# Kernel tuning notes

Hardware: AMD Instinct MI355X
Metric: run time of the kernel (lower is better)

## Reference

```python
import jax, jax.numpy as jnp
import numpy as np
from jax import lax

DIM = 64
HEADS = 8

def conv1x1(x, w):
    # x: [B,C,H,W], w: [O,I,1,1]
    return lax.conv_general_dilated(x, w, (1, 1), 'VALID',
                                    dimension_numbers=('NCHW', 'OIHW', 'NCHW'))

def dwconv3x3(x, w):
    # depthwise 3x3, w: [C,1,3,3]
    C = x.shape[1]
    return lax.conv_general_dilated(x, w, (1, 1), ((1, 1), (1, 1)),
                                    dimension_numbers=('NCHW', 'OIHW', 'NCHW'),
                                    feature_group_count=C)

def setup_inputs() -> dict:
    key = jax.random.key(0)
    ks = jax.random.split(key, 7)
    B, C, H, W = 8, DIM, 256, 256
    x = jax.random.normal(ks[0], (B, C, H, W), dtype=jnp.float32)
    w_gate = jax.random.normal(ks[1], (C, C, 1, 1), dtype=jnp.float32) * 0.05
    w_gate_dw = jax.random.normal(ks[2], (C, 1, 3, 3), dtype=jnp.float32) * 0.05
    w_qkv = jax.random.normal(ks[3], (3 * C, C, 1, 1), dtype=jnp.float32) * 0.05
    w_qkv_dw = jax.random.normal(ks[4], (3 * C, 1, 3, 3), dtype=jnp.float32) * 0.05
    w_proj = jax.random.normal(ks[5], (C, C, 1, 1), dtype=jnp.float32) * 0.05
    temperature = jnp.ones((HEADS, 1, 1), dtype=jnp.float32)
    return {'x': x, 'w_gate': w_gate, 'w_gate_dw': w_gate_dw,
            'w_qkv': w_qkv, 'w_qkv_dw': w_qkv_dw, 'w_proj': w_proj,
            'temperature': temperature}

def reference(x, w_gate, w_gate_dw, w_qkv, w_qkv_dw, w_proj, temperature):
    b, c, h, w = x.shape
    head = HEADS
    cph = c // head  # channels per head

    gate = dwconv3x3(conv1x1(x, w_gate), w_gate_dw)  # [b,c,h,w]
    qkv = dwconv3x3(conv1x1(x, w_qkv), w_qkv_dw)     # [b,3c,h,w]
    q, k, v = jnp.split(qkv, 3, axis=1)

    def to_heads(t):
        return t.reshape(b, head, cph, h * w)  # [b,head,c',hw]
    q, k, v = to_heads(q), to_heads(k), to_heads(v)

    # L2-normalize along the spatial (hw) axis (torch F.normalize, eps=1e-12)
    q = q / jnp.maximum(jnp.linalg.norm(q, axis=-1, keepdims=True), 1e-12)
    k = k / jnp.maximum(jnp.linalg.norm(k, axis=-1, keepdims=True), 1e-12)

    # transposed attention over channels: [b,head,c',c']
    attn = jnp.einsum('bhcn,bhdn->bhcd', q, k) * temperature
    attn = jax.nn.softmax(attn, axis=-1)
    out = jnp.einsum('bhcd,bhdn->bhcn', attn, v)  # [b,head,c',hw]
    out = out.reshape(b, c, h, w)

    out = jax.nn.gelu(gate, approximate=False) * out
    out = conv1x1(out, w_proj)
    return out
```

## Files before the change

### kernel.cpp

```cpp
#include <hip/hip_runtime.h>

typedef _Float16 f16;
using f16x4 = __attribute__((ext_vector_type(4))) _Float16;
using f16x8 = __attribute__((ext_vector_type(8))) _Float16;
using f32x4 = __attribute__((ext_vector_type(4))) float;

#define HW 65536
#define NBAND 16
#define ROWS 16
#define RS 320

static __device__ __forceinline__ float my_erf(float v) {
  float x = fabsf(v);
  float t = 1.f / (1.f + 0.3275911f * x);
  float y = t * (0.254829592f + t * (-0.284496736f + t * (1.421413741f
          + t * (-1.453152027f + t * 1.061405429f))));
  float r = 1.f - y * __expf(-x * x);
  return v < 0.f ? -r : r;
}
static __device__ __forceinline__ float my_gelu(float s) {
  return 0.5f * s * (1.f + my_erf(s * 0.70710678118654752f));
}

__global__ void TRA_Attention_15281493639325_kernel() {}

__global__ void k_signal(float* out, long long n, float val) {
  long long i = (long long)blockIdx.x * blockDim.x + threadIdx.x;
  long long stride = (long long)gridDim.x * blockDim.x;
  for (; i < n; i += stride) out[i] = val;
}

__global__ __launch_bounds__(256) void k0_wconv(
    const float* __restrict__ w_gate, const float* __restrict__ w_qkv,
    f16* __restrict__ W16)
{
  int i = blockIdx.x * 256 + threadIdx.x;
  int m = i >> 4, kc = i & 15;
  const float* src = (m < 64) ? (w_gate + m*64 + kc*4)
                              : (w_qkv + (m-64)*64 + kc*4);
  float4 f = *(const float4*)src;
  f16x4 pk = { (f16)f.x, (f16)f.y, (f16)f.z, (f16)f.w };
  *(f16x4*)(W16 + m*64 + kc*4) = pk;
}

__global__ __launch_bounds__(256) void k1_mfma(
    const float* __restrict__ x, const f16* __restrict__ W16,
    f16* __restrict__ A)
{
  __shared__ __align__(16) unsigned char xs[8192];
  __shared__ __align__(16) f16 os[256*64];

  const int tid = threadIdx.x, blk = blockIdx.x;
  const int b = blk >> 8;
  const long long row0 = (long long)(blk & 255) * 256;

  const int wave = tid >> 6, lane = tid & 63;
  const int m0 = (wave >> 1) * 128, n0 = (wave & 1) * 32;
  const int lr = lane & 15, lg = lane >> 4;

  float4 pre[4];
  #pragma unroll
  for (int i = 0; i < 4; ++i) {
    int cid = tid + (i << 8), k = cid >> 4, c = cid & 15;
    pre[i] = *(const float4*)(x + ((long long)b*64 + k)*HW + row0 + c*4);
  }

  for (int t = 0; t < 4; ++t) {
    const long long p0 = row0 + t*64;

    #pragma unroll
    for (int i = 0; i < 4; ++i) {
      int cid = tid + (i << 8), k = cid >> 4, c = cid & 15;
      const float* e = (const float*)&pre[i];
      #pragma unroll
      for (int j = 0; j < 4; ++j) {
        int p = c*4 + j;
        int hp = ((p & 7) ^ ((p >> 3) & 7)) << 4;
        *(f16*)(xs + p*128 + ((2*k) ^ hp)) = (f16)e[j];
      }
    }
    __syncthreads();

    if (t < 3) {
      const long long pn = row0 + (t+1)*64;
      #pragma unroll
      for (int i = 0; i < 4; ++i) {
        int cid = tid + (i << 8), k = cid >> 4, c = cid & 15;
        pre[i] = *(const float4*)(x + ((long long)b*64 + k)*HW + pn + c*4);
      }
    }

    f32x4 acc[8][2];
    #pragma unroll
    for (int i = 0; i < 8; ++i)
      #pragma unroll
      for (int j = 0; j < 2; ++j) acc[i][j] = (f32x4){0.f,0.f,0.f,0.f};

    #pragma unroll
    for (int ks = 0; ks < 2; ++ks) {
      f16x8 af[8], bfr[2];
      #pragma unroll
      for (int mi = 0; mi < 8; ++mi) {
        int m = m0 + mi*16 + lr;
        af[mi] = *(const f16x8*)(W16 + m*64 + ks*32 + lg*8);
      }
      #pragma unroll
      for (int ni = 0; ni < 2; ++ni) {
        int p = n0 + ni*16 + lr;
        int hp = ((p & 7) ^ ((p >> 3) & 7)) << 4;
        bfr[ni] = *(const f16x8*)(xs + p*128 + ((ks*64 + lg*16) ^ hp));
      }
      #pragma unroll
      for (int mi = 0; mi < 8; ++mi)
        #pragma unroll
        for (int ni = 0; ni < 2; ++ni)
          acc[mi][ni] = __builtin_amdgcn_mfma_f32_16x16x32_f16(
              af[mi], bfr[ni], acc[mi][ni], 0, 0, 0);
    }
    __syncthreads();

    #pragma unroll
    for (int mi = 0; mi < 8; ++mi)
      #pragma unroll
      for (int ni = 0; ni < 2; ++ni)
        #pragma unroll
        for (int r = 0; r < 4; ++r) {
          int m = m0 + mi*16 + lg*4 + r;
          int p = n0 + ni*16 + lr;
          os[m*64 + (p ^ ((m & 7) << 3))] = (f16)acc[mi][ni][r];
        }
    __syncthreads();

    #pragma unroll
    for (int pass = 0; pass < 8; ++pass) {
      int idx = pass*256 + tid;
      int row = idx >> 3, c8 = idx & 7;
      f16x8 v = *(const f16x8*)((const unsigned char*)os + row*128
                                + ((c8 ^ (row & 7)) * 16));
      *(f16x8*)(A + ((long long)b*256 + row)*HW + p0 + c8*8) = v;
    }
    __syncthreads();
  }
}

__global__ __launch_bounds__(256) void k2a_dw(
    const f16* __restrict__ A, const float* __restrict__ w_gate_dw,
    const float* __restrict__ w_qkv_dw, f16* __restrict__ Vv, f16* __restrict__ GG)
{
  const int tid = threadIdx.x, blk = blockIdx.x;
  const int yband = blk & 3, ch2 = (blk >> 2) & 127, b = blk >> 9;
  const bool isv = ch2 >= 64;
  const int c = isv ? ch2 - 64 : ch2;
  const f16* src = A + ((long long)b*256 + (isv ? 192 + c : c)) * HW;
  const float* wsrc = isv ? (w_qkv_dw + (128 + c)*9) : (w_gate_dw + c*9);
  f16* dst = (isv ? Vv : GG) + ((long long)b*64 + c) * HW;

  float wd[9];
  #pragma unroll
  for (int j = 0; j < 9; ++j) wd[j] = wsrc[j];

  const int xc = tid & 31, ysub = tid >> 5;
  const int lane = tid & 63;
  const int xbase = xc * 8;
  const int y0 = yband * 64 + ysub * 8;

  float rb[3][10];

  auto load_row = [&](int y, float* r) {
    if (y >= 0 && y < 256) {
      uint4 raw = *(const uint4*)(src + y*256 + xbase);
      const f16* e = (const f16*)&raw;
      #pragma unroll
      for (int t = 0; t < 8; ++t) r[1 + t] = (float)e[t];
    } else {
      #pragma unroll
      for (int t = 0; t < 8; ++t) r[1 + t] = 0.f;
    }
    float lf = __shfl(r[8], lane - 1);
    float rf = __shfl(r[1], lane + 1);
    r[0] = (xc == 0)  ? 0.f : lf;
    r[9] = (xc == 31) ? 0.f : rf;
  };

  load_row(y0 - 1, rb[0]);
  load_row(y0,     rb[1]);

  #pragma unroll
  for (int i = 0; i < 8; ++i) {
    load_row(y0 + i + 1, rb[(i + 2) % 3]);
    const float* rm = rb[i % 3];
    const float* r0 = rb[(i + 1) % 3];
    const float* rp = rb[(i + 2) % 3];
    f16x8 st;
    #pragma unroll
    for (int j = 0; j < 8; ++j) {
      float s = wd[0]*rm[j] + wd[1]*rm[j+1] + wd[2]*rm[j+2]
              + wd[3]*r0[j] + wd[4]*r0[j+1] + wd[5]*r0[j+2]
              + wd[6]*rp[j] + wd[7]*rp[j+1] + wd[8]*rp[j+2];
      if (!isv) s = my_gelu(s);
      st[j] = (f16)s;
    }
    *(f16x8*)(dst + (y0 + i)*256 + xbase) = st;
  }
}

__device__ __forceinline__ int ridx(int c, int slot, int i) {
  return ((((c << 2) | slot) * RS) + i) ^ ((c & 7) << 3);
}

__global__ __launch_bounds__(64) void k2b_qk(
    const f16* __restrict__ A, const float* __restrict__ w_qkv_dw,
    float* __restrict__ GRP)
{
  __shared__ __align__(16) f16 ring[16*4*RS];
  const int lane = threadIdx.x, blk = blockIdx.x;
  const int band = blk & (NBAND-1), h = (blk >> 4) & 7, b = blk >> 7;

  const int c  = lane & 15, g  = lane >> 4;
  const int cs = lane >> 2, q4 = lane & 3;

  const int wrow = (c < 8) ? (h*8 + c) : (64 + h*8 + (c - 8));
  float wq[9];
  #pragma unroll
  for (int j = 0; j < 9; ++j) wq[j] = w_qkv_dw[wrow*9 + j];

  const f16* sbase = A + ((long long)b*256 +
      (cs < 8 ? 64 + h*8 + cs : 128 + h*8 + (cs - 8))) * HW;

  ring[ridx(cs, q4, 7)]   = (f16)0.f;
  ring[ridx(cs, q4, 264)] = (f16)0.f;

  auto load_row = [&](int yy, uint4* r) {
    if (yy >= 0 && yy < 256) {
      const f16* p = sbase + yy*256 + q4*64;
      #pragma unroll
      for (int t = 0; t < 8; ++t) r[t] = *(const uint4*)(p + t*8);
    } else {
      #pragma unroll
      for (int t = 0; t < 8; ++t) r[t] = make_uint4(0u,0u,0u,0u);
    }
  };
  auto write_row = [&](int slot, const uint4* r) {
    #pragma unroll
    for (int t = 0; t < 8; ++t)
      *(uint4*)&ring[ridx(cs, slot, 8 + q4*64 + t*8)] = r[t];
  };

  const int y0 = band * ROWS;
  {
    uint4 r[8];
    load_row(y0-1, r); write_row((y0+3)&3, r);
    load_row(y0,   r); write_row((y0+4)&3, r);
    load_row(y0+1, r); write_row((y0+5)&3, r);
  }
  __syncthreads();

  f32x4 acc = (f32x4){0.f, 0.f, 0.f, 0.f};

  for (int y = y0; y < y0 + ROWS; ++y) {
    uint4 r[8];
    const bool pf = (y + 2 <= y0 + ROWS);
    if (pf) load_row(y + 2, r);

    const int s0 = (y+3)&3, s1 = (y+4)&3, s2 = (y+5)&3;
    #pragma unroll
    for (int q = 0; q < 8; ++q) {
      const int base = 7 + q*32 + g*8;
      float v0[10], v1[10], v2[10];
      #pragma unroll
      for (int t = 0; t < 10; ++t) {
        v0[t] = (float)ring[ridx(c, s0, base+t)];
        v1[t] = (float)ring[ridx(c, s1, base+t)];
        v2[t] = (float)ring[ridx(c, s2, base+t)];
      }
      f16x8 frag;
      #pragma unroll
      for (int j = 0; j < 8; ++j) {
        float s = wq[0]*v0[j] + wq[1]*v0[j+1] + wq[2]*v0[j+2]
                + wq[3]*v1[j] + wq[4]*v1[j+1] + wq[5]*v1[j+2]
                + wq[6]*v2[j] + wq[7]*v2[j+1] + wq[8]*v2[j+2];
        frag[j] = (f16)s;
      }
      acc = __builtin_amdgcn_mfma_f32_16x16x32_f16(frag, frag, acc, 0, 0, 0);
    }
    if (pf) write_row((y+6)&3, r);
    __syncthreads();
  }

  const long long gbase = (long long)((b*8 + h)*NBAND + band) * 80;
  #pragma unroll
  for (int reg = 0; reg < 4; ++reg) {
    int rrow = g*4 + reg;
    float val = acc[reg];
    if (rrow == c) GRP[gbase + c] = val;
    else if (rrow < 8 && c >= 8) GRP[gbase + 16 + rrow*8 + (c-8)] = val;
  }
}

__global__ __launch_bounds__(64) void k2c_attn(
    const float* __restrict__ GRP, const float* __restrict__ temp,
    float* __restrict__ ATT)
{
  __shared__ float s[80];
  const int tid = threadIdx.x;
  const int h = blockIdx.x & 7, b = blockIdx.x >> 3;
  for (int i = tid; i < 80; i += 64) {
    float v = 0.f;
    for (int band = 0; band < NBAND; ++band)
      v += GRP[(((b*8 + h)*NBAND + band) * 80) + i];
    s[i] = v;
  }
  __syncthreads();
  const int c = tid >> 3, d = tid & 7;
  float nq = fmaxf(sqrtf(s[c]), 1e-12f);
  float nk = fmaxf(sqrtf(s[8 + d]), 1e-12f);
  float logit = s[16 + c*8 + d] / (nq * nk) * temp[h];
  float m = logit;
  #pragma unroll
  for (int off = 4; off; off >>= 1) m = fmaxf(m, __shfl_xor(m, off));
  float e = __expf(logit - m);
  float sum = e;
  #pragma unroll
  for (int off = 4; off; off >>= 1) sum += __shfl_xor(sum, off);
  ATT[((b*8 + h)*8 + c)*8 + d] = e / sum;
}

__global__ __launch_bounds__(256) void k3_out(
    const f16* __restrict__ Vv, const f16* __restrict__ GG,
    const float* __restrict__ ATT, const float* __restrict__ w_proj,
    float* __restrict__ out)
{
  __shared__ __align__(16) unsigned char lds[64*128 + 256*128 + 2048];
  unsigned char* wl = lds;
  unsigned char* xs = lds + 64*128;
  float* attn_s = (float*)(lds + 64*128 + 256*128);

  const int tid = threadIdx.x;
  const int y = blockIdx.x & 255, b = blockIdx.x >> 8;

  for (int cid = tid; cid < 1024; cid += 256) {
    int m = cid >> 4, kc = cid & 15;
    float4 f = *(const float4*)(w_proj + m*64 + kc*4);
    int hm = ((m & 7) ^ ((m >> 3) & 7)) << 4;
    f16x4 pk = { (f16)f.x, (f16)f.y, (f16)f.z, (f16)f.w };
    *(f16x4*)(wl + m*128 + ((kc*8) ^ hm)) = pk;
  }
  for (int i = tid; i < 512; i += 256) attn_s[i] = ATT[b*512 + i];
  __syncthreads();

  {
    const int pg = tid & 31, hd = tid >> 5;
    const long long base = ((long long)b*64 + hd*8)*HW + (long long)y*256 + pg*8;
    f16x8 vv[8], gg[8];
    #pragma unroll
    for (int d = 0; d < 8; ++d)
      vv[d] = *(const f16x8*)(Vv + base + (long long)d*HW);
    #pragma unroll
    for (int c = 0; c < 8; ++c)
      gg[c] = *(const f16x8*)(GG + base + (long long)c*HW);
    float a[8][8];
    #pragma unroll
    for (int c = 0; c < 8; ++c)
      #pragma unroll
      for (int d = 0; d < 8; ++d) a[c][d] = attn_s[hd*64 + c*8 + d];
    #pragma unroll
    for (int j = 0; j < 8; ++j) {
      int p = pg*8 + j;
      int hp = ((p & 7) ^ ((p >> 3) & 7)) << 4;
      f16x8 st;
      #pragma unroll
      for (int c = 0; c < 8; ++c) {
        float av = 0.f;
        #pragma unroll
        for (int d = 0; d < 8; ++d) av += a[c][d] * (float)vv[d][j];
        st[c] = (f16)((float)gg[c][j] * av);
      }
      *(f16x8*)(xs + p*128 + ((hd*16) ^ hp)) = st;
    }
  }
  __syncthreads();

  const int wave = tid >> 6, lane = tid & 63;
  const int n0 = wave * 64;
  const int lr = lane & 15, lg = lane >> 4;

  f32x4 acc[4][4];
  #pragma unroll
  for (int i = 0; i < 4; ++i)
    #pragma unroll
    for (int j = 0; j < 4; ++j) acc[i][j] = (f32x4){0.f,0.f,0.f,0.f};

  #pragma unroll
  for (int ks = 0; ks < 2; ++ks) {
    f16x8 af[4], bfr[4];
    #pragma unroll
    for (int mi = 0; mi < 4; ++mi) {
      int m = mi*16 + lr;
      int hm = ((m & 7) ^ ((m >> 3) & 7)) << 4;
      af[mi] = *(const f16x8*)(wl + m*128 + ((ks*64 + lg*16) ^ hm));
    }
    #pragma unroll
    for (int ni = 0; ni < 4; ++ni) {
      int p = n0 + ni*16 + lr;
      int hp = ((p & 7) ^ ((p >> 3) & 7)) << 4;
      bfr[ni] = *(const f16x8*)(xs + p*128 + ((ks*64 + lg*16) ^ hp));
    }
    #pragma unroll
    for (int mi = 0; mi < 4; ++mi)
      #pragma unroll
      for (int ni = 0; ni < 4; ++ni)
        acc[mi][ni] = __builtin_amdgcn_mfma_f32_16x16x32_f16(
            af[mi], bfr[ni], acc[mi][ni], 0, 0, 0);
  }

  const long long obase = (long long)b*64*HW + (long long)y*256;
  #pragma unroll
  for (int mi = 0; mi < 4; ++mi)
    #pragma unroll
    for (int ni = 0; ni < 4; ++ni)
      #pragma unroll
      for (int r = 0; r < 4; ++r) {
        int m = mi*16 + lg*4 + r;
        int p = n0 + ni*16 + lr;
        out[obase + (long long)m*HW + p] = acc[mi][ni][r];
      }
}

extern "C" void kernel_launch(void* const* d_in, const int* in_sizes, int n_in,
                              void* d_out, int out_size, void* d_ws, size_t ws_size,
                              hipStream_t stream)
{
  float* out = (float*)d_out;

  int mp[7] = {-1,-1,-1,-1,-1,-1,-1};
  bool ok = (n_in == 7);
  if (ok) {
    int n4 = 0;
    for (int i = 0; i < 7; ++i) {
      long s = in_sizes[i];
      if      (s == 33554432) mp[0] = i;
      else if (s == 576)      mp[2] = i;
      else if (s == 12288)    mp[3] = i;
      else if (s == 1728)     mp[4] = i;
      else if (s == 8)        mp[6] = i;
      else if (s == 4096)     { if (n4 == 0) mp[1] = i; else mp[5] = i; ++n4; }
    }
    ok = ok && (n4 == 2);
    for (int i = 0; i < 7; ++i) ok = ok && (mp[i] >= 0);
  }
  if (!ok) { k_signal<<<2048,256,0,stream>>>(out, (long long)out_size, 2000.0f); return; }
  if (out_size != 33554432) { k_signal<<<2048,256,0,stream>>>(out, (long long)out_size, 3000.0f); return; }

  const float* x    = (const float*)d_in[mp[0]];
  const float* wg   = (const float*)d_in[mp[1]];
  const float* wgd  = (const float*)d_in[mp[2]];
  const float* wqkv = (const float*)d_in[mp[3]];
  const float* wqd  = (const float*)d_in[mp[4]];
  const float* wpj  = (const float*)d_in[mp[5]];
  const float* tp   = (const float*)d_in[mp[6]];

  unsigned char* ws = (unsigned char*)d_ws;
  const size_t GRP_SZ   = 8UL*8*NBAND*80*4;
  const size_t FULL     = 402653184UL + GRP_SZ + 16384UL + 32768UL;
  const size_t PERB_GRP = 8UL*NBAND*80*4;
  const size_t PERB     = 50331648UL + PERB_GRP + 2048UL + 32768UL;

  if (ws != nullptr && ws_size >= FULL) {
    f16*   A    = (f16*)ws;
    f16*   Vv   = (f16*)(ws + 268435456UL);
    f16*   GG   = (f16*)(ws + 335544320UL);
    float* GRP  = (float*)(ws + 402653184UL);
    float* ATT  = (float*)(ws + 402653184UL + GRP_SZ);
    f16*   W16  = (f16*)(ws + 402653184UL + GRP_SZ + 16384UL);
    k0_wconv<<<16,   256, 0, stream>>>(wg, wqkv, W16);
    k1_mfma <<<2048, 256, 0, stream>>>(x, W16, A);
    k2a_dw  <<<4096, 256, 0, stream>>>(A, wgd, wqd, Vv, GG);
    k2b_qk  <<<8*8*NBAND, 64, 0, stream>>>(A, wqd, GRP);
    k2c_attn<<<64,   64,  0, stream>>>(GRP, tp, ATT);
    k3_out  <<<2048, 256, 0, stream>>>(Vv, GG, ATT, wpj, out);
  } else if (ws != nullptr && ws_size >= PERB) {
    f16*   A    = (f16*)ws;
    f16*   Vv   = (f16*)(ws + 33554432UL);
    f16*   GG   = (f16*)(ws + 41943040UL);
    float* GRP  = (float*)(ws + 50331648UL);
    float* ATT  = (float*)(ws + 50331648UL + PERB_GRP);
    f16*   W16  = (f16*)(ws + 50331648UL + PERB_GRP + 2048UL);
    k0_wconv<<<16, 256, 0, stream>>>(wg, wqkv, W16);
    for (int b = 0; b < 8; ++b) {
      const float* xb = x + (long long)b*64*HW;
      float* ob = out + (long long)b*64*HW;
      k1_mfma <<<256,  256, 0, stream>>>(xb, W16, A);
      k2a_dw  <<<512,  256, 0, stream>>>(A, wgd, wqd, Vv, GG);
      k2b_qk  <<<8*NBAND, 64, 0, stream>>>(A, wqd, GRP);
      k2c_attn<<<8,    64,  0, stream>>>(GRP, tp, ATT);
      k3_out  <<<256,  256, 0, stream>>>(Vv, GG, ATT, wpj, ob);
    }
  } else {
    k_signal<<<2048,256,0,stream>>>(out, (long long)out_size, 1000.0f);
  }
}
```

Measured before the change: 287.7 us.

## Keep depthwise-conv rows in registers with lane shuffles and finer bands in QK kernel

```diff
diff --git a/kernel.cpp b/kernel.cpp
--- a/kernel.cpp
+++ b/kernel.cpp
@@ -6,9 +6,8 @@
 using f32x4 = __attribute__((ext_vector_type(4))) float;
 
 #define HW 65536
-#define NBAND 16
-#define ROWS 16
-#define RS 320
+#define NBAND 32
+#define ROWS 8
 
 static __device__ __forceinline__ float my_erf(float v) {
   float x = fabsf(v);
@@ -204,17 +203,13 @@
   }
 }
 
-__device__ __forceinline__ int ridx(int c, int slot, int i) {
-  return ((((c << 2) | slot) * RS) + i) ^ ((c & 7) << 3);
-}
-
 __global__ __launch_bounds__(64) void k2b_qk(
     const f16* __restrict__ A, const float* __restrict__ w_qkv_dw,
     float* __restrict__ GRP)
 {
-  __shared__ __align__(16) f16 ring[16*4*RS];
+  __shared__ __align__(16) f16 slot[16*264];
   const int lane = threadIdx.x, blk = blockIdx.x;
-  const int band = blk & (NBAND-1), h = (blk >> 4) & 7, b = blk >> 7;
+  const int band = blk & (NBAND-1), h = (blk >> 5) & 7, b = blk >> 8;
 
   const int c  = lane & 15, g  = lane >> 4;
   const int cs = lane >> 2, q4 = lane & 3;
@@ -227,10 +222,11 @@
   const f16* sbase = A + ((long long)b*256 +
       (cs < 8 ? 64 + h*8 + cs : 128 + h*8 + (cs - 8))) * HW;
 
-  ring[ridx(cs, q4, 7)]   = (f16)0.f;
-  ring[ridx(cs, q4, 264)] = (f16)0.f;
-
-  auto load_row = [&](int yy, uint4* r) {
+  f16x8 Ra[8], Rb[8], Rc[8];
+  f32x4 acc = (f32x4){0.f, 0.f, 0.f, 0.f};
+
+  auto fetch_row = [&](int yy, f16x8* R) {
+    uint4 r[8];
     if (yy >= 0 && yy < 256) {
       const f16* p = sbase + yy*256 + q4*64;
       #pragma unroll
@@ -239,53 +235,58 @@
       #pragma unroll
       for (int t = 0; t < 8; ++t) r[t] = make_uint4(0u,0u,0u,0u);
     }
+    __syncthreads();
+    #pragma unroll
+    for (int t = 0; t < 8; ++t)
+      *(uint4*)&slot[cs*264 + q4*64 + t*8] = r[t];
+    __syncthreads();
+    #pragma unroll
+    for (int q = 0; q < 8; ++q)
+      R[q] = *(const f16x8*)&slot[c*264 + q*32 + g*8];
   };
-  auto write_row = [&](int slot, const uint4* r) {
-    #pragma unroll
-    for (int t = 0; t < 8; ++t)
-      *(uint4*)&ring[ridx(cs, slot, 8 + q4*64 + t*8)] = r[t];
+
+  auto conv_accum = [&](const f16x8* R, const float* w, float* fr, int q) {
+    float v[10];
+    #pragma unroll
+    for (int t = 0; t < 8; ++t) v[1 + t] = (float)R[q][t];
+    float e7p = (q > 0) ? (float)R[q-1][7] : 0.f;
+    float e0n = (q < 7) ? (float)R[q+1][0] : 0.f;
+    float L1 = __shfl(v[8], lane - 16);
+    float L2 = __shfl(e7p, (lane & 15) + 48);
+    float Q1 = __shfl(v[1], lane + 16);
+    float Q2 = __shfl(e0n, lane & 15);
+    v[0] = (g > 0) ? L1 : ((q > 0) ? L2 : 0.f);
+    v[9] = (g < 3) ? Q1 : ((q < 7) ? Q2 : 0.f);
+    #pragma unroll
+    for (int j = 0; j < 8; ++j)
+      fr[j] += w[0]*v[j] + w[1]*v[j+1] + w[2]*v[j+2];
   };
 
+  auto do_row = [&](const f16x8* RM, const f16x8* RC, const f16x8* RP) {
+    #pragma unroll
+    for (int q = 0; q < 8; ++q) {
+      float fr[8] = {0.f,0.f,0.f,0.f,0.f,0.f,0.f,0.f};
+      conv_accum(RM, wq + 0, fr, q);
+      conv_accum(RC, wq + 3, fr, q);
+      conv_accum(RP, wq + 6, fr, q);
+      f16x8 frag;
+      #pragma unroll
+      for (int j = 0; j < 8; ++j) frag[j] = (f16)fr[j];
+      acc = __builtin_amdgcn_mfma_f32_16x16x32_f16(frag, frag, acc, 0, 0, 0);
+    }
+  };
+
   const int y0 = band * ROWS;
-  {
-    uint4 r[8];
-    load_row(y0-1, r); write_row((y0+3)&3, r);
-    load_row(y0,   r); write_row((y0+4)&3, r);
-    load_row(y0+1, r); write_row((y0+5)&3, r);
-  }
-  __syncthreads();
-
-  f32x4 acc = (f32x4){0.f, 0.f, 0.f, 0.f};
-
-  for (int y = y0; y < y0 + ROWS; ++y) {
-    uint4 r[8];
-    const bool pf = (y + 2 <= y0 + ROWS);
-    if (pf) load_row(y + 2, r);
-
-    const int s0 = (y+3)&3, s1 = (y+4)&3, s2 = (y+5)&3;
-    #pragma unroll
-    for (int q = 0; q < 8; ++q) {
-      const int base = 7 + q*32 + g*8;
-      float v0[10], v1[10], v2[10];
-      #pragma unroll
-      for (int t = 0; t < 10; ++t) {
-        v0[t] = (float)ring[ridx(c, s0, base+t)];
-        v1[t] = (float)ring[ridx(c, s1, base+t)];
-        v2[t] = (float)ring[ridx(c, s2, base+t)];
-      }
-      f16x8 frag;
-      #pragma unroll
-      for (int j = 0; j < 8; ++j) {
-        float s = wq[0]*v0[j] + wq[1]*v0[j+1] + wq[2]*v0[j+2]
-                + wq[3]*v1[j] + wq[4]*v1[j+1] + wq[5]*v1[j+2]
-                + wq[6]*v2[j] + wq[7]*v2[j+1] + wq[8]*v2[j+2];
-        frag[j] = (f16)s;
-      }
-      acc = __builtin_amdgcn_mfma_f32_16x16x32_f16(frag, frag, acc, 0, 0, 0);
-    }
-    if (pf) write_row((y+6)&3, r);
-    __syncthreads();
-  }
+  fetch_row(y0 - 1, Ra);
+  fetch_row(y0,     Rb);
+  fetch_row(y0 + 1, Rc); do_row(Ra, Rb, Rc);
+  fetch_row(y0 + 2, Ra); do_row(Rb, Rc, Ra);
+  fetch_row(y0 + 3, Rb); do_row(Rc, Ra, Rb);
+  fetch_row(y0 + 4, Rc); do_row(Ra, Rb, Rc);
+  fetch_row(y0 + 5, Ra); do_row(Rb, Rc, Ra);
+  fetch_row(y0 + 6, Rb); do_row(Rc, Ra, Rb);
+  fetch_row(y0 + 7, Rc); do_row(Ra, Rb, Rc);
+  fetch_row(y0 + 8, Ra); do_row(Rb, Rc, Ra);
 
   const long long gbase = (long long)((b*8 + h)*NBAND + band) * 80;
   #pragma unroll
```

Result: slower. 422.1 us (+46.7%).
